# Kernel tuning notes

Hardware: AMD Instinct MI355X
Metric: run time of the kernel (lower is better)

Reference implementation:

```python
import jax, jax.numpy as jnp
import numpy as np

B, T, DM, H, DH, P = 8, 512, 1024, 16, 64, 3584


def rotate_half(x):
    x1, x2 = x[..., : x.shape[-1] // 2], x[..., x.shape[-1] // 2 :]
    return jnp.concatenate([-x2, x1], axis=-1)


def setup_inputs() -> dict:
    key = jax.random.key(0)
    ks = jax.random.split(key, 16)
    x_new = jax.random.normal(ks[0], (B, T, DM), dtype=jnp.float32)
    # realistic RoPE tables for positions [P, P+T)
    inv_freq = 1.0 / (10000.0 ** (jnp.arange(0, DH, 2, dtype=jnp.float32) / DH))
    pos = jnp.arange(P, P + T, dtype=jnp.float32)
    freqs = pos[:, None] * inv_freq[None, :]  # [T, DH/2]
    emb = jnp.concatenate([freqs, freqs], axis=-1)  # [T, DH]
    rotary_cos = jnp.cos(emb)[None, None]  # [1,1,T,DH]
    rotary_sin = jnp.sin(emb)[None, None]
    past_k = jax.random.normal(ks[1], (B, H, P, DH), dtype=jnp.float32)
    past_v = jax.random.normal(ks[2], (B, H, P, DH), dtype=jnp.float32)
    past_lengths = jax.random.randint(ks[3], (B,), 0, P + 1, dtype=jnp.int32)
    new_token_counts = jax.random.randint(ks[4], (B,), 1, T + 1, dtype=jnp.int32)
    valid_new_mask = jnp.arange(T)[None, :] < new_token_counts[:, None]  # [B,T] bool
    s = 0.02
    Wq = jax.random.normal(ks[5], (DM, DM), dtype=jnp.float32) * s
    Wk = jax.random.normal(ks[6], (DM, DM), dtype=jnp.float32) * s
    Wv = jax.random.normal(ks[7], (DM, DM), dtype=jnp.float32) * s
    Wo = jax.random.normal(ks[8], (DM, DM), dtype=jnp.float32) * s
    bq = jax.random.normal(ks[9], (DM,), dtype=jnp.float32) * s
    bk = jax.random.normal(ks[10], (DM,), dtype=jnp.float32) * s
    bv = jax.random.normal(ks[11], (DM,), dtype=jnp.float32) * s
    bo = jax.random.normal(ks[12], (DM,), dtype=jnp.float32) * s
    return dict(x_new=x_new, rotary_cos=rotary_cos, rotary_sin=rotary_sin,
                past_k=past_k, past_v=past_v, past_lengths=past_lengths,
                valid_new_mask=valid_new_mask, new_token_counts=new_token_counts,
                Wq=Wq, bq=bq, Wk=Wk, bk=bk, Wv=Wv, bv=bv, Wo=Wo, bo=bo)


def reference(x_new, rotary_cos, rotary_sin, past_k, past_v, past_lengths,
              valid_new_mask, new_token_counts, Wq, bq, Wk, bk, Wv, bv, Wo, bo):
    b, t, _ = x_new.shape
    # projections -> [B,H,T,DH]
    def proj(W, bias):
        y = x_new @ W + bias
        return y.reshape(b, t, H, DH).transpose(0, 2, 1, 3)
    q = proj(Wq, bq)
    k_new = proj(Wk, bk)
    v_new = proj(Wv, bv)
    # RoPE on q and new keys
    cos = rotary_cos.astype(q.dtype)
    sin = rotary_sin.astype(q.dtype)
    q = q * cos + rotate_half(q) * sin
    k_new = k_new * cos + rotate_half(k_new) * sin
    # zero out padded new tokens (applied to q, k_new, v_new as in original)
    vmask = valid_new_mask[:, None, :, None].astype(q.dtype)
    q = q * vmask
    k_new = k_new * vmask
    v_new = v_new * vmask
    # trim/mask past cache per sample
    trimmed_past = jnp.clip(past_lengths, 0, P)
    pmask = (jnp.arange(P)[None, :] < trimmed_past[:, None])[:, None, :, None].astype(q.dtype)
    pk = past_k.astype(q.dtype) * pmask
    pv = past_v.astype(q.dtype) * pmask
    k_total = jnp.concatenate([pk, k_new], axis=2)  # [B,H,P+T,DH]
    v_total = jnp.concatenate([pv, v_new], axis=2)
    total_lengths = trimmed_past + new_token_counts  # [B]
    # key validity mask over concatenated axis: positions < total_lengths
    valid_keys = jnp.arange(P + t)[None, :] < total_lengths[:, None]  # [B,S]
    scale = 1.0 / jnp.sqrt(jnp.asarray(DH, dtype=q.dtype))
    scores = jnp.einsum('bhqd,bhkd->bhqk', q, k_total) * scale  # [B,H,T,S]
    neg = jnp.asarray(-1e9, dtype=scores.dtype)
    scores = jnp.where(valid_keys[:, None, None, :], scores, neg)
    attn = jax.nn.softmax(scores, axis=-1)
    out = jnp.einsum('bhqk,bhkd->bhqd', attn, v_total)  # [B,H,T,DH]
    out = out.transpose(0, 2, 1, 3).reshape(b, t, DM)
    out = out @ Wo + bo
    out = out * valid_new_mask[:, :, None].astype(out.dtype)
    return out
```

## Files before the change

### kernel.cpp

```cpp
#include <hip/hip_runtime.h>


typedef unsigned short u16;
typedef unsigned int   u32;
typedef float  f32x4  __attribute__((ext_vector_type(4)));
typedef __bf16 bf16x8 __attribute__((ext_vector_type(8)));

#define DEV static __device__ __forceinline__

constexpr int NP = 3584;

DEV u16 bf16rn(float f){
  u32 u = __float_as_uint(f);
  return (u16)((u + 0x7fffu + ((u >> 16) & 1u)) >> 16);
}
DEV float bf2f(u16 h){ return __uint_as_float((u32)h << 16); }
DEV void split2(float f, u16 &h, u16 &l){ h = bf16rn(f); l = bf16rn(f - bf2f(h)); }

DEV f32x4 mfma16(bf16x8 a, bf16x8 b, f32x4 c){
  return __builtin_amdgcn_mfma_f32_16x16x32_bf16(a, b, c, 0, 0, 0);
}

DEV ushort4 cvt4(float4 v){
  ushort4 h; h.x=bf16rn(v.x); h.y=bf16rn(v.y); h.z=bf16rn(v.z); h.w=bf16rn(v.w); return h;
}

DEV void gload_lds16(const u16* g, u16* l){
  __builtin_amdgcn_global_load_lds((const __attribute__((address_space(1))) void*)g,
                                   (__attribute__((address_space(3))) void*)l, 16, 0, 0);
}

__global__ __launch_bounds__(256) void k_split_x(const float* __restrict__ x,
                                                 u16* __restrict__ xh, u16* __restrict__ xl){
  int i = blockIdx.x * 256 + threadIdx.x;
  float4 v = ((const float4*)x)[i];
  u16 h0,l0,h1,l1,h2,l2,h3,l3;
  split2(v.x,h0,l0); split2(v.y,h1,l1); split2(v.z,h2,l2); split2(v.w,h3,l3);
  ushort4 hv; hv.x=h0; hv.y=h1; hv.z=h2; hv.w=h3;
  ushort4 lv; lv.x=l0; lv.y=l1; lv.z=l2; lv.w=l3;
  ((ushort4*)xh)[i] = hv; ((ushort4*)xl)[i] = lv;
}

__global__ __launch_bounds__(256) void k_wsplit(const float* __restrict__ w0, const float* __restrict__ w1,
                                                const float* __restrict__ w2, const float* __restrict__ w3,
                                                u16* __restrict__ Wth, u16* __restrict__ Wtl){
  __shared__ float tl[64][65];
  int z = blockIdx.z;
  const float* W = (z==0) ? w0 : (z==1) ? w1 : (z==2) ? w2 : w3;
  u16* oh = Wth + (size_t)z * (1024*1024);
  u16* ol = Wtl + (size_t)z * (1024*1024);
  int n0 = blockIdx.x*64, k0 = blockIdx.y*64;
  int tid = threadIdx.x;
  #pragma unroll
  for (int i=0;i<16;++i){
    int idx = i*256 + tid; int rr = idx >> 6, cc = idx & 63;
    tl[rr][cc] = W[(size_t)(k0+rr)*1024 + n0 + cc];
  }
  __syncthreads();
  #pragma unroll
  for (int i=0;i<16;++i){
    int idx = i*256 + tid; int rr = idx >> 6, cc = idx & 63;
    u16 h,l; split2(tl[cc][rr], h, l);
    size_t o = (size_t)(n0+rr)*1024 + k0 + cc;
    oh[o] = h; ol[o] = l;
  }
}

__global__ __launch_bounds__(256) void k_qkv(
    const u16* __restrict__ xh, const u16* __restrict__ xl,
    const u16* __restrict__ Wth, const u16* __restrict__ Wtl,
    const float* __restrict__ bq, const float* __restrict__ bk, const float* __restrict__ bv,
    const float* __restrict__ rcos, const float* __restrict__ rsin,
    const int* __restrict__ cnts,
    u16* __restrict__ qh, u16* __restrict__ ql,
    u16* __restrict__ knt, u16* __restrict__ vnt)
{
  int zi = blockIdx.z;
  int n0 = blockIdx.x * 128, m0 = blockIdx.y * 128;
  int b = m0 >> 9, t0 = m0 & 511;
  int cnt = cnts[b];
  if (t0 >= cnt) return;
  const u16* Bh = Wth + (size_t)zi * (1024*1024);
  const u16* Bl = Wtl + (size_t)zi * (1024*1024);
  const float* bias = (zi==0) ? bq : (zi==1) ? bk : bv;

  __shared__ u16 sA[2][128*40];
  __shared__ u16 sB[2][128*40];

  int tid = threadIdx.x, lane = tid & 63, wid = tid >> 6;
  int r = lane & 15, quad = lane >> 4;
  int wm = (wid >> 1) * 64, wn = (wid & 1) * 64;

  const f32x4 fz = {0.f,0.f,0.f,0.f};
  f32x4 acc[4][4];
  #pragma unroll
  for (int i=0;i<4;++i){
    #pragma unroll
    for (int j=0;j<4;++j) acc[i][j] = fz;
  }

  int srow = tid >> 2, sc8 = (tid & 3) * 8;

  for (int kt = 0; kt < 32; ++kt){
    int kb = kt * 32;
    __syncthreads();
    {
      size_t ga  = (size_t)(m0 + srow) * 1024 + kb + sc8;
      size_t gb  = (size_t)(n0 + srow) * 1024 + kb + sc8;
      int lo = srow*40 + sc8, lo2 = lo + 64*40;
      *(uint4*)&sA[0][lo]  = *(const uint4*)&xh[ga];
      *(uint4*)&sA[1][lo]  = *(const uint4*)&xl[ga];
      *(uint4*)&sB[0][lo]  = *(const uint4*)&Bh[gb];
      *(uint4*)&sB[1][lo]  = *(const uint4*)&Bl[gb];
      *(uint4*)&sA[0][lo2] = *(const uint4*)&xh[ga + 64*1024];
      *(uint4*)&sA[1][lo2] = *(const uint4*)&xl[ga + 64*1024];
      *(uint4*)&sB[0][lo2] = *(const uint4*)&Bh[gb + 64*1024];
      *(uint4*)&sB[1][lo2] = *(const uint4*)&Bl[gb + 64*1024];
    }
    __syncthreads();
    bf16x8 ah[4], al[4], bh8[4], bl8[4];
    #pragma unroll
    for (int mf=0; mf<4; ++mf){
      int off = (wm + mf*16 + r)*40 + quad*8;
      ah[mf] = *(const bf16x8*)&sA[0][off];
      al[mf] = *(const bf16x8*)&sA[1][off];
    }
    #pragma unroll
    for (int nf=0; nf<4; ++nf){
      int off = (wn + nf*16 + r)*40 + quad*8;
      bh8[nf] = *(const bf16x8*)&sB[0][off];
      bl8[nf] = *(const bf16x8*)&sB[1][off];
    }
    #pragma unroll
    for (int mf=0; mf<4; ++mf){
      #pragma unroll
      for (int nf=0; nf<4; ++nf){
        acc[mf][nf] = mfma16(ah[mf], bh8[nf], acc[mf][nf]);
        acc[mf][nf] = mfma16(al[mf], bh8[nf], acc[mf][nf]);
        acc[mf][nf] = mfma16(ah[mf], bl8[nf], acc[mf][nf]);
      }
    }
  }

  float vals[4][4][4];
  #pragma unroll
  for (int mf=0;mf<4;++mf){
    #pragma unroll
    for (int nf=0;nf<4;++nf){
      float bb = bias[n0 + wn + nf*16 + r];
      #pragma unroll
      for (int e=0;e<4;++e) vals[mf][nf][e] = acc[mf][nf][e] + bb;
    }
  }
  if (zi < 2){
    #pragma unroll
    for (int mf=0;mf<4;++mf){
      #pragma unroll
      for (int e=0;e<4;++e){
        int t = t0 + wm + mf*16 + quad*4 + e;
        #pragma unroll
        for (int nf=0;nf<2;++nf){
          int d = nf*16 + r;
          float c1 = rcos[t*64 + d],      s1 = rsin[t*64 + d];
          float c2 = rcos[t*64 + d + 32], s2 = rsin[t*64 + d + 32];
          float x1 = vals[mf][nf][e], x2 = vals[mf][nf+2][e];
          vals[mf][nf][e]   = x1*c1 - x2*s1;
          vals[mf][nf+2][e] = x2*c2 + x1*s2;
        }
      }
    }
  }
  #pragma unroll
  for (int mf=0;mf<4;++mf){
    #pragma unroll
    for (int e=0;e<4;++e){
      int t = t0 + wm + mf*16 + quad*4 + e;
      float msk = (t < cnt) ? 1.f : 0.f;
      #pragma unroll
      for (int nf=0;nf<4;++nf){
        int gc = n0 + wn + nf*16 + r;
        int head = gc >> 6, d = gc & 63;
        float v = vals[mf][nf][e] * msk;
        u16 hh, ll; split2(v, hh, ll);
        size_t bh8t = (size_t)(b*16 + head)*8;
        if (zi == 0){
          size_t o = ((size_t)(b*16 + head)*512 + t)*64 + d;
          qh[o] = hh; ql[o] = ll;
        } else if (zi == 1){
          size_t o = ((bh8t + (t>>6))*64 + (t&63))*64 + (d ^ ((t&7)<<3));
          knt[o] = hh;
        } else {
          size_t o = ((bh8t + (t>>6))*64 + d)*64 + ((t&63) ^ ((d&7)<<3));
          vnt[o] = hh;
        }
      }
    }
  }
}

__global__ __launch_bounds__(256) void k_conv(
    const float* __restrict__ pk, const float* __restrict__ pv,
    const int* __restrict__ plen,
    u16* __restrict__ ckh, u16* __restrict__ cvt)
{
  int t = blockIdx.x, h = blockIdx.y, b = blockIdx.z;
  int Lp = min(max(plen[b], 0), NP);
  int jend = min(((Lp + 63) >> 6) << 6, NP);
  if (t*64 >= jend) return;
  int tid = threadIdx.x;
  int bh = b*16 + h;
  int row = tid >> 2, cg = (tid & 3) * 16;
  int jj = t*64 + row;
  size_t src = ((size_t)bh*NP + jj)*64;

  __shared__ float tl[64][65];

  float4 kv4[4], vv4[4];
  #pragma unroll
  for (int i=0;i<4;++i){
    kv4[i] = *(const float4*)&pk[src + cg + i*4];
    vv4[i] = *(const float4*)&pv[src + cg + i*4];
  }
  if (jj >= Lp){
    float4 z4 = {0.f,0.f,0.f,0.f};
    #pragma unroll
    for (int i=0;i<4;++i){ kv4[i]=z4; vv4[i]=z4; }
  }
  size_t kdst = ((size_t)bh*NP + jj)*64;
  #pragma unroll
  for (int i=0;i<4;++i){
    int c4 = cg + i*4;
    *(ushort4*)&ckh[kdst + (c4 ^ ((jj&7)<<3))] = cvt4(kv4[i]);
  }
  #pragma unroll
  for (int i=0;i<4;++i){
    tl[row][cg+i*4+0] = vv4[i].x;
    tl[row][cg+i*4+1] = vv4[i].y;
    tl[row][cg+i*4+2] = vv4[i].z;
    tl[row][cg+i*4+3] = vv4[i].w;
  }
  __syncthreads();
  int d = tid >> 2, jg = (tid & 3) * 16;
  size_t vdst = (((size_t)bh*56 + t)*64 + d)*64;
  #pragma unroll
  for (int i=0;i<4;++i){
    int j4 = jg + i*4;
    ushort4 hv;
    hv.x = bf16rn(tl[j4+0][d]);
    hv.y = bf16rn(tl[j4+1][d]);
    hv.z = bf16rn(tl[j4+2][d]);
    hv.w = bf16rn(tl[j4+3][d]);
    *(ushort4*)&cvt[vdst + (j4 ^ ((d&7)<<3))] = hv;
  }
}

__global__ __launch_bounds__(256,3) void k_attn(
    const u16* __restrict__ qh_, const u16* __restrict__ ql_,
    const u16* __restrict__ knt, const u16* __restrict__ vnt,
    const u16* __restrict__ ckh, const u16* __restrict__ cvt,
    const int* __restrict__ plen, const int* __restrict__ cnts,
    int S, float* __restrict__ pl, float* __restrict__ pO)
{
  int qt = blockIdx.x, h = blockIdx.y;
  int zb = blockIdx.z;
  int b = zb / S, s = zb - b * S;
  int cnt = cnts[b];
  int q0 = qt * 128;
  if (q0 >= cnt) return;
  int Lp = min(max(plen[b], 0), NP);
  int TL = Lp + cnt;
  int Ln = max(0, TL - NP);
  int jend = min(((Lp + 63) >> 6) << 6, NP);
  int minTLP = min(TL, NP);
  int Zar = max(0, minTLP - jend);
  int npast = jend >> 6, nnew = (Ln + 63) >> 6;
  int Tt = npast + nnew;
  int TLu = min(TL, jend) + Ln;
  int qsp = (Tt + S - 1) / S;
  int it0 = s * qsp, it1 = min(Tt, it0 + qsp);
  bool hasZ = (s == 0 && Zar > 0);
  if (it0 >= it1 && !hasZ) return;

  __shared__ __align__(16) u16 sK [2][4096];
  __shared__ __align__(16) u16 sVT[2][4096];
  __shared__ __align__(16) u16 sP [4][2048];

  int tid = threadIdx.x, lane = tid & 63, wid = tid >> 6;
  int r = lane & 15, quad = lane >> 4;
  int wm0 = wid * 32;
  int bh = b*16 + h;

  bf16x8 Qh[2][2], Ql[2][2];
  size_t qbase = ((size_t)bh*512 + q0 + wm0) * 64;
  #pragma unroll
  for (int mf=0;mf<2;++mf){
    #pragma unroll
    for (int ks=0;ks<2;++ks){
      size_t o = qbase + (size_t)(mf*16 + r)*64 + ks*32 + quad*8;
      Qh[mf][ks] = *(const bf16x8*)&qh_[o];
      Ql[mf][ks] = *(const bf16x8*)&ql_[o];
    }
  }

  const f32x4 fz = {0.f,0.f,0.f,0.f};
  f32x4 O[2][4];
  float lsum[2][4];
  #pragma unroll
  for (int mf=0;mf<2;++mf){
    #pragma unroll
    for (int e=0;e<4;++e) lsum[mf][e] = 0.f;
    #pragma unroll
    for (int nf=0;nf<4;++nf) O[mf][nf] = fz;
  }

  const float kscale = 0.125f * 1.44269504088896340736f;
  int ub = wid * 512;

  auto stage = [&](int pp, int it){
    const u16* ks; const u16* vs;
    if (it < npast){
      ks = ckh + ((size_t)bh*NP + (size_t)it*64)*64;
      vs = cvt + ((size_t)bh*56 + it)*4096;
    } else {
      ks = knt + ((size_t)bh*8 + (it - npast))*4096;
      vs = vnt + ((size_t)bh*8 + (it - npast))*4096;
    }
    gload_lds16(ks + ub + lane*8,        &sK [pp][ub]);
    gload_lds16(ks + ub + 2048 + lane*8, &sK [pp][ub + 2048]);
    gload_lds16(vs + ub + lane*8,        &sVT[pp][ub]);
    gload_lds16(vs + ub + 2048 + lane*8, &sVT[pp][ub + 2048]);
  };

  int p = 0;
  if (it0 < it1) stage(0, it0);
  __syncthreads();

  for (int it = it0; it < it1; ++it){
    if (it + 1 < it1) stage(p^1, it + 1);

    f32x4 Sc[2][4];
    #pragma unroll
    for (int mf=0;mf<2;++mf){
      #pragma unroll
      for (int jf=0;jf<4;++jf) Sc[mf][jf] = fz;
    }
    #pragma unroll
    for (int ks=0;ks<2;++ks){
      #pragma unroll
      for (int jf=0;jf<4;++jf){
        int jr = jf*16 + r;
        int off = jr*64 + ((ks*32 + quad*8) ^ ((jr&7)<<3));
        bf16x8 kbh = *(const bf16x8*)&sK[p][off];
        #pragma unroll
        for (int mf=0;mf<2;++mf){
          Sc[mf][jf] = mfma16(Qh[mf][ks], kbh, Sc[mf][jf]);
          Sc[mf][jf] = mfma16(Ql[mf][ks], kbh, Sc[mf][jf]);
        }
      }
    }

    int jlim = TLu - it*64;
    #pragma unroll
    for (int mf=0;mf<2;++mf){
      #pragma unroll
      for (int e=0;e<4;++e){
        int row = mf*16 + quad*4 + e;
        int sw = ((row>>2)&7) << 3;
        float ls = 0.f;
        #pragma unroll
        for (int jf=0;jf<4;++jf){
          float sv = Sc[mf][jf][e] * kscale - 4.0f;
          sv = (jf*16 + r < jlim) ? sv : -3.0e38f;
          float pj = exp2f(sv);
          ls += pj;
          __bf16 pb = (__bf16)pj;
          sP[wid][row*64 + ((jf*16 + r) ^ sw)] = __builtin_bit_cast(u16, pb);
        }
        lsum[mf][e] += ls;
      }
    }
    __syncthreads();

    #pragma unroll
    for (int ks=0;ks<2;++ks){
      bf16x8 pah[2];
      #pragma unroll
      for (int mf=0;mf<2;++mf){
        int row = mf*16 + r;
        pah[mf] = *(const bf16x8*)&sP[wid][row*64 + ((ks*32 + quad*8) ^ (((row>>2)&7)<<3))];
      }
      #pragma unroll
      for (int nf=0;nf<4;++nf){
        int d = nf*16 + r;
        bf16x8 vbh = *(const bf16x8*)&sVT[p][d*64 + ((ks*32 + quad*8) ^ ((d&7)<<3))];
        #pragma unroll
        for (int mf=0;mf<2;++mf){
          O[mf][nf] = mfma16(pah[mf], vbh, O[mf][nf]);
        }
      }
    }
    __syncthreads();
    p ^= 1;
  }

  int pidx = ((b*16 + h)*4 + qt)*S + s;
  float* plr = pl + (size_t)pidx*128;
  float* po  = pO + (size_t)pidx*8192;
  float zadd = (s == 0) ? (float)Zar * 0.0625f : 0.f;
  #pragma unroll
  for (int mf=0;mf<2;++mf){
    #pragma unroll
    for (int e=0;e<4;++e){
      int row = wm0 + mf*16 + quad*4 + e;
      float l = lsum[mf][e];
      l += __shfl_xor(l, 1);
      l += __shfl_xor(l, 2);
      l += __shfl_xor(l, 4);
      l += __shfl_xor(l, 8);
      if (r == 0) plr[row] = l + zadd;
      #pragma unroll
      for (int nf=0;nf<4;++nf) po[row*64 + nf*16 + r] = O[mf][nf][e];
    }
  }
}

__global__ __launch_bounds__(256) void k_reduce(
    const float* __restrict__ pl, const float* __restrict__ pO,
    const int* __restrict__ plen, const int* __restrict__ cnts,
    int S, u16* __restrict__ aoh, u16* __restrict__ aol)
{
  int qt = blockIdx.x, h = blockIdx.y, b = blockIdx.z;
  int cnt = cnts[b]; int q0 = qt*128;
  if (q0 >= cnt) return;
  int Lp = min(max(plen[b], 0), NP);
  int TL = Lp + cnt;
  int Ln = max(0, TL - NP);
  int jend = min(((Lp + 63) >> 6) << 6, NP);
  int minTLP = min(TL, NP);
  int Zar = max(0, minTLP - jend);
  int npast = jend >> 6, nnew = (Ln + 63) >> 6;
  int Tt = npast + nnew;
  int qsp = (Tt + S - 1) / S;

  int tid = threadIdx.x;
  int row = tid >> 1, c0 = (tid & 1) * 32;
  int base = ((b*16 + h)*4 + qt)*S;

  float L = 0.f;
  float acc[32];
  #pragma unroll
  for (int i=0;i<32;++i) acc[i] = 0.f;
  for (int s2=0;s2<S;++s2){
    bool act = (s2*qsp < Tt) || (s2 == 0 && Zar > 0);
    if (!act) continue;
    L += pl[(size_t)(base+s2)*128 + row];
    const float4* po = (const float4*)(pO + (size_t)(base+s2)*8192 + row*64 + c0);
    #pragma unroll
    for (int i=0;i<8;++i){
      float4 v = po[i];
      acc[4*i+0] += v.x; acc[4*i+1] += v.y; acc[4*i+2] += v.z; acc[4*i+3] += v.w;
    }
  }
  float inv = 1.f / L;
  size_t o = ((size_t)b*512 + q0 + row)*1024 + h*64 + c0;
  #pragma unroll
  for (int i=0;i<8;++i){
    ushort4 hv, lv;
    u16 hh, ll;
    split2(acc[4*i+0]*inv, hh, ll); hv.x=hh; lv.x=ll;
    split2(acc[4*i+1]*inv, hh, ll); hv.y=hh; lv.y=ll;
    split2(acc[4*i+2]*inv, hh, ll); hv.z=hh; lv.z=ll;
    split2(acc[4*i+3]*inv, hh, ll); hv.w=hh; lv.w=ll;
    *(ushort4*)&aoh[o + 4*i] = hv;
    *(ushort4*)&aol[o + 4*i] = lv;
  }
}

__global__ __launch_bounds__(256) void k_oproj(
    const u16* __restrict__ ah_, const u16* __restrict__ al_,
    const u16* __restrict__ Wth, const u16* __restrict__ Wtl,
    const float* __restrict__ bo, const int* __restrict__ cnts,
    float* __restrict__ out)
{
  int n0 = blockIdx.x * 128, m0 = blockIdx.y * 128;
  int b = m0 >> 9, t0 = m0 & 511;
  int cnt = cnts[b];
  int tid = threadIdx.x;
  if (t0 >= cnt){
    float4 z4 = {0.f,0.f,0.f,0.f};
    #pragma unroll
    for (int i=0;i<16;++i){
      int v = tid + i*256;
      int row = v >> 5, c4 = (v & 31) * 4;
      *(float4*)&out[(size_t)(m0+row)*1024 + n0 + c4] = z4;
    }
    return;
  }
  const u16* Bh = Wth + 3ull*1024*1024;
  const u16* Bl = Wtl + 3ull*1024*1024;

  __shared__ u16 sA[2][128*40];
  __shared__ u16 sB[2][128*40];

  int lane = tid & 63, wid = tid >> 6;
  int r = lane & 15, quad = lane >> 4;
  int wm = (wid >> 1) * 64, wn = (wid & 1) * 64;

  const f32x4 fz = {0.f,0.f,0.f,0.f};
  f32x4 acc[4][4];
  #pragma unroll
  for (int i=0;i<4;++i){
    #pragma unroll
    for (int j=0;j<4;++j) acc[i][j] = fz;
  }

  int srow = tid >> 2, sc8 = (tid & 3) * 8;

  for (int kt = 0; kt < 32; ++kt){
    int kb = kt * 32;
    __syncthreads();
    {
      size_t ga  = (size_t)(m0 + srow) * 1024 + kb + sc8;
      size_t gb  = (size_t)(n0 + srow) * 1024 + kb + sc8;
      int lo = srow*40 + sc8, lo2 = lo + 64*40;
      *(uint4*)&sA[0][lo]  = *(const uint4*)&ah_[ga];
      *(uint4*)&sA[1][lo]  = *(const uint4*)&al_[ga];
      *(uint4*)&sB[0][lo]  = *(const uint4*)&Bh[gb];
      *(uint4*)&sB[1][lo]  = *(const uint4*)&Bl[gb];
      *(uint4*)&sA[0][lo2] = *(const uint4*)&ah_[ga + 64*1024];
      *(uint4*)&sA[1][lo2] = *(const uint4*)&al_[ga + 64*1024];
      *(uint4*)&sB[0][lo2] = *(const uint4*)&Bh[gb + 64*1024];
      *(uint4*)&sB[1][lo2] = *(const uint4*)&Bl[gb + 64*1024];
    }
    __syncthreads();
    bf16x8 ah8[4], al8[4], bh8[4], bl8[4];
    #pragma unroll
    for (int mf=0; mf<4; ++mf){
      int off = (wm + mf*16 + r)*40 + quad*8;
      ah8[mf] = *(const bf16x8*)&sA[0][off];
      al8[mf] = *(const bf16x8*)&sA[1][off];
    }
    #pragma unroll
    for (int nf=0; nf<4; ++nf){
      int off = (wn + nf*16 + r)*40 + quad*8;
      bh8[nf] = *(const bf16x8*)&sB[0][off];
      bl8[nf] = *(const bf16x8*)&sB[1][off];
    }
    #pragma unroll
    for (int mf=0; mf<4; ++mf){
      #pragma unroll
      for (int nf=0; nf<4; ++nf){
        acc[mf][nf] = mfma16(ah8[mf], bh8[nf], acc[mf][nf]);
        acc[mf][nf] = mfma16(al8[mf], bh8[nf], acc[mf][nf]);
        acc[mf][nf] = mfma16(ah8[mf], bl8[nf], acc[mf][nf]);
      }
    }
  }

  #pragma unroll
  for (int mf=0;mf<4;++mf){
    #pragma unroll
    for (int e=0;e<4;++e){
      int t = t0 + wm + mf*16 + quad*4 + e;
      float msk = (t < cnt) ? 1.f : 0.f;
      int row = m0 + wm + mf*16 + quad*4 + e;
      #pragma unroll
      for (int nf=0;nf<4;++nf){
        int gc = n0 + wn + nf*16 + r;
        out[(size_t)row*1024 + gc] = (acc[mf][nf][e] + bo[gc]) * msk;
      }
    }
  }
}

extern "C" void kernel_launch(void* const* d_in, const int* in_sizes, int n_in,
                              void* d_out, int out_size, void* d_ws, size_t ws_size,
                              hipStream_t stream) {
  (void)in_sizes; (void)n_in; (void)out_size;
  const float* x    = (const float*)d_in[0];
  const float* rcos = (const float*)d_in[1];
  const float* rsin = (const float*)d_in[2];
  const float* pk   = (const float*)d_in[3];
  const float* pv   = (const float*)d_in[4];
  const int*   plen = (const int*)d_in[5];
  const int*   cnts = (const int*)d_in[7];
  const float* Wq = (const float*)d_in[8];
  const float* bq = (const float*)d_in[9];
  const float* Wk = (const float*)d_in[10];
  const float* bk = (const float*)d_in[11];
  const float* Wv = (const float*)d_in[12];
  const float* bv = (const float*)d_in[13];
  const float* Wo = (const float*)d_in[14];
  const float* bo = (const float*)d_in[15];
  float* out = (float*)d_out;

  char* w = (char*)d_ws;
  const size_t MB = 1ull << 20;
  u16* Wth = (u16*)(w + 0*MB);
  u16* Wtl = (u16*)(w + 8*MB);
  u16* qh  = (u16*)(w + 16*MB);
  u16* ql  = (u16*)(w + 24*MB);
  u16* knt = (u16*)(w + 32*MB);
  u16* vnt = (u16*)(w + 40*MB);
  u16* ckh = (u16*)(w + 48*MB);
  u16* xh  = (u16*)(w + 48*MB);
  u16* xl  = (u16*)(w + 56*MB);
  u16* cvt = (u16*)(w + 104*MB);
  float* pl = (float*)(w + 160*MB);
  float* pO = (float*)(w + 162*MB);
  u16* aoh = xh;
  u16* aol = xl;

  int S = (int)((ws_size - 162*MB) / (16*MB));
  if (S > 8) S = 8;
  if (S < 1) S = 1;

  k_split_x<<<dim3(4096), dim3(256), 0, stream>>>(x, xh, xl);
  k_wsplit<<<dim3(16,16,4), dim3(256), 0, stream>>>(Wq, Wk, Wv, Wo, Wth, Wtl);
  k_qkv<<<dim3(8,32,3), dim3(256), 0, stream>>>(xh, xl, Wth, Wtl, bq, bk, bv,
                                                rcos, rsin, cnts,
                                                qh, ql, knt, vnt);
  k_conv<<<dim3(56,16,8), dim3(256), 0, stream>>>(pk, pv, plen, ckh, cvt);
  k_attn<<<dim3(4,16,8*S), dim3(256), 0, stream>>>(qh, ql, knt, vnt, ckh, cvt,
                                                   plen, cnts, S, pl, pO);
  k_reduce<<<dim3(4,16,8), dim3(256), 0, stream>>>(pl, pO, plen, cnts, S, aoh, aol);
  k_oproj<<<dim3(8,32), dim3(256), 0, stream>>>(aoh, aol, Wth, Wtl, bo, cnts, out);
}
```

Baseline: 583.5 us.

## Double-buffer QKV and output-projection GEMMs with direct global-to-LDS loads and block swizzle

The QKV and output-projection GEMM kernels now stage tiles with direct global-to-LDS loads (gload_lds16) into double-buffered shared memory. The next K tile is prefetched while MFMAs run on the current one, cutting the loop to one barrier per iteration. Block indices are remapped so neighbouring blocks share A/B tiles for better L2 reuse, and launch bounds request 2 blocks per CU. The unpadded 32-element LDS rows may cause bank conflicts on fragment reads, and gload_lds16 is assumed to be defined in the hidden part of the file.

Measured after the change: 554.2 us. -5.0%, faster.

```diff
diff --git a/kernel.cpp b/kernel.cpp
--- a/kernel.cpp
+++ b/kernel.cpp
@@ -66,7 +66,7 @@
   }
 }
 
-__global__ __launch_bounds__(256) void k_qkv(
+__global__ __launch_bounds__(256,2) void k_qkv(
     const u16* __restrict__ xh, const u16* __restrict__ xl,
     const u16* __restrict__ Wth, const u16* __restrict__ Wtl,
     const float* __restrict__ bq, const float* __restrict__ bk, const float* __restrict__ bv,
@@ -76,7 +76,9 @@
     u16* __restrict__ knt, u16* __restrict__ vnt)
 {
   int zi = blockIdx.z;
-  int n0 = blockIdx.x * 128, m0 = blockIdx.y * 128;
+  int bx = blockIdx.x, by = blockIdx.y;
+  int n0 = ((bx & 3)*2 + (by & 1)) * 128;
+  int m0 = ((bx >> 2)*16 + (by >> 1)) * 128;
   int b = m0 >> 9, t0 = m0 & 511;
   int cnt = cnts[b];
   if (t0 >= cnt) return;
@@ -84,8 +86,8 @@
   const u16* Bl = Wtl + (size_t)zi * (1024*1024);
   const float* bias = (zi==0) ? bq : (zi==1) ? bk : bv;
 
-  __shared__ u16 sA[2][128*40];
-  __shared__ u16 sB[2][128*40];
+  __shared__ __align__(16) u16 sA[2][2][4096];
+  __shared__ __align__(16) u16 sB[2][2][4096];
 
   int tid = threadIdx.x, lane = tid & 63, wid = tid >> 6;
   int r = lane & 15, quad = lane >> 4;
@@ -99,47 +101,52 @@
     for (int j=0;j<4;++j) acc[i][j] = fz;
   }
 
-  int srow = tid >> 2, sc8 = (tid & 3) * 8;
+  int sc = wid * 2;
+
+  auto stage = [&](int p, int kt){
+    int kb = kt * 32;
+    #pragma unroll
+    for (int c=0;c<2;++c){
+      int s   = (sc + c)*64 + lane;
+      int row = s >> 2;
+      int cg8 = (s & 3) * 8;
+      size_t ga = (size_t)(m0 + row)*1024 + kb + cg8;
+      size_t gb = (size_t)(n0 + row)*1024 + kb + cg8;
+      int lo = (sc + c)*512;
+      gload_lds16(&xh[ga], &sA[p][0][lo]);
+      gload_lds16(&xl[ga], &sA[p][1][lo]);
+      gload_lds16(&Bh[gb], &sB[p][0][lo]);
+      gload_lds16(&Bl[gb], &sB[p][1][lo]);
+    }
+  };
+
+  stage(0, 0);
+  __syncthreads();
 
   for (int kt = 0; kt < 32; ++kt){
-    int kb = kt * 32;
+    int cur = kt & 1;
+    if (kt + 1 < 32) stage(cur ^ 1, kt + 1);
+
+    bf16x8 ah[4], al[4];
+    #pragma unroll
+    for (int mf=0; mf<4; ++mf){
+      int off = (wm + mf*16 + r)*32 + quad*8;
+      ah[mf] = *(const bf16x8*)&sA[cur][0][off];
+      al[mf] = *(const bf16x8*)&sA[cur][1][off];
+    }
+    #pragma unroll
+    for (int nf=0; nf<4; ++nf){
+      int off = (wn + nf*16 + r)*32 + quad*8;
+      bf16x8 bh8 = *(const bf16x8*)&sB[cur][0][off];
+      bf16x8 bl8 = *(const bf16x8*)&sB[cur][1][off];
+      #pragma unroll
+      for (int mf=0; mf<4; ++mf){
+        acc[mf][nf] = mfma16(ah[mf], bh8, acc[mf][nf]);
+        acc[mf][nf] = mfma16(al[mf], bh8, acc[mf][nf]);
+        acc[mf][nf] = mfma16(ah[mf], bl8, acc[mf][nf]);
+      }
+    }
     __syncthreads();
-    {
-      size_t ga  = (size_t)(m0 + srow) * 1024 + kb + sc8;
-      size_t gb  = (size_t)(n0 + srow) * 1024 + kb + sc8;
-      int lo = srow*40 + sc8, lo2 = lo + 64*40;
-      *(uint4*)&sA[0][lo]  = *(const uint4*)&xh[ga];
-      *(uint4*)&sA[1][lo]  = *(const uint4*)&xl[ga];
-      *(uint4*)&sB[0][lo]  = *(const uint4*)&Bh[gb];
-      *(uint4*)&sB[1][lo]  = *(const uint4*)&Bl[gb];
-      *(uint4*)&sA[0][lo2] = *(const uint4*)&xh[ga + 64*1024];
-      *(uint4*)&sA[1][lo2] = *(const uint4*)&xl[ga + 64*1024];
-      *(uint4*)&sB[0][lo2] = *(const uint4*)&Bh[gb + 64*1024];
-      *(uint4*)&sB[1][lo2] = *(const uint4*)&Bl[gb + 64*1024];
-    }
-    __syncthreads();
-    bf16x8 ah[4], al[4], bh8[4], bl8[4];
-    #pragma unroll
-    for (int mf=0; mf<4; ++mf){
-      int off = (wm + mf*16 + r)*40 + quad*8;
-      ah[mf] = *(const bf16x8*)&sA[0][off];
-      al[mf] = *(const bf16x8*)&sA[1][off];
-    }
-    #pragma unroll
-    for (int nf=0; nf<4; ++nf){
-      int off = (wn + nf*16 + r)*40 + quad*8;
-      bh8[nf] = *(const bf16x8*)&sB[0][off];
-      bl8[nf] = *(const bf16x8*)&sB[1][off];
-    }
-    #pragma unroll
-    for (int mf=0; mf<4; ++mf){
-      #pragma unroll
-      for (int nf=0; nf<4; ++nf){
-        acc[mf][nf] = mfma16(ah[mf], bh8[nf], acc[mf][nf]);
-        acc[mf][nf] = mfma16(al[mf], bh8[nf], acc[mf][nf]);
-        acc[mf][nf] = mfma16(ah[mf], bl8[nf], acc[mf][nf]);
-      }
-    }
   }
 
   float vals[4][4][4];
@@ -476,13 +483,15 @@
   }
 }
 
-__global__ __launch_bounds__(256) void k_oproj(
+__global__ __launch_bounds__(256,2) void k_oproj(
     const u16* __restrict__ ah_, const u16* __restrict__ al_,
     const u16* __restrict__ Wth, const u16* __restrict__ Wtl,
     const float* __restrict__ bo, const int* __restrict__ cnts,
     float* __restrict__ out)
 {
-  int n0 = blockIdx.x * 128, m0 = blockIdx.y * 128;
+  int bx = blockIdx.x, by = blockIdx.y;
+  int n0 = ((bx & 3)*2 + (by & 1)) * 128;
+  int m0 = ((bx >> 2)*16 + (by >> 1)) * 128;
   int b = m0 >> 9, t0 = m0 & 511;
   int cnt = cnts[b];
   int tid = threadIdx.x;
@@ -499,8 +508,8 @@
   const u16* Bh = Wth + 3ull*1024*1024;
   const u16* Bl = Wtl + 3ull*1024*1024;
 
-  __shared__ u16 sA[2][128*40];
-  __shared__ u16 sB[2][128*40];
+  __shared__ __align__(16) u16 sA[2][2][4096];
+  __shared__ __align__(16) u16 sB[2][2][4096];
 
   int lane = tid & 63, wid = tid >> 6;
   int r = lane & 15, quad = lane >> 4;
@@ -514,47 +523,52 @@
     for (int j=0;j<4;++j) acc[i][j] = fz;
   }
 
-  int srow = tid >> 2, sc8 = (tid & 3) * 8;
+  int sc = wid * 2;
+
+  auto stage = [&](int p, int kt){
+    int kb = kt * 32;
+    #pragma unroll
+    for (int c=0;c<2;++c){
+      int s   = (sc + c)*64 + lane;
+      int row = s >> 2;
+      int cg8 = (s & 3) * 8;
+      size_t ga = (size_t)(m0 + row)*1024 + kb + cg8;
+      size_t gb = (size_t)(n0 + row)*1024 + kb + cg8;
+      int lo = (sc + c)*512;
+      gload_lds16(&ah_[ga], &sA[p][0][lo]);
+      gload_lds16(&al_[ga], &sA[p][1][lo]);
+      gload_lds16(&Bh[gb],  &sB[p][0][lo]);
+      gload_lds16(&Bl[gb],  &sB[p][1][lo]);
+    }
+  };
+
+  stage(0, 0);
+  __syncthreads();
 
   for (int kt = 0; kt < 32; ++kt){
-    int kb = kt * 32;
+    int cur = kt & 1;
+    if (kt + 1 < 32) stage(cur ^ 1, kt + 1);
+
+    bf16x8 ah8[4], al8[4];
+    #pragma unroll
+    for (int mf=0; mf<4; ++mf){
+      int off = (wm + mf*16 + r)*32 + quad*8;
+      ah8[mf] = *(const bf16x8*)&sA[cur][0][off];
+      al8[mf] = *(const bf16x8*)&sA[cur][1][off];
+    }
+    #pragma unroll
+    for (int nf=0; nf<4; ++nf){
+      int off = (wn + nf*16 + r)*32 + quad*8;
+      bf16x8 bh8 = *(const bf16x8*)&sB[cur][0][off];
+      bf16x8 bl8 = *(const bf16x8*)&sB[cur][1][off];
+      #pragma unroll
+      for (int mf=0; mf<4; ++mf){
+        acc[mf][nf] = mfma16(ah8[mf], bh8, acc[mf][nf]);
+        acc[mf][nf] = mfma16(al8[mf], bh8, acc[mf][nf]);
+        acc[mf][nf] = mfma16(ah8[mf], bl8, acc[mf][nf]);
+      }
+    }
     __syncthreads();
-    {
-      size_t ga  = (size_t)(m0 + srow) * 1024 + kb + sc8;
-      size_t gb  = (size_t)(n0 + srow) * 1024 + kb + sc8;
-      int lo = srow*40 + sc8, lo2 = lo + 64*40;
-      *(uint4*)&sA[0][lo]  = *(const uint4*)&ah_[ga];
-      *(uint4*)&sA[1][lo]  = *(const uint4*)&al_[ga];
-      *(uint4*)&sB[0][lo]  = *(const uint4*)&Bh[gb];
-      *(uint4*)&sB[1][lo]  = *(const uint4*)&Bl[gb];
-      *(uint4*)&sA[0][lo2] = *(const uint4*)&ah_[ga + 64*1024];
-      *(uint4*)&sA[1][lo2] = *(const uint4*)&al_[ga + 64*1024];
-      *(uint4*)&sB[0][lo2] = *(const uint4*)&Bh[gb + 64*1024];
-      *(uint4*)&sB[1][lo2] = *(const uint4*)&Bl[gb + 64*1024];
-    }
-    __syncthreads();
-    bf16x8 ah8[4], al8[4], bh8[4], bl8[4];
-    #pragma unroll
-    for (int mf=0; mf<4; ++mf){
-      int off = (wm + mf*16 + r)*40 + quad*8;
-      ah8[mf] = *(const bf16x8*)&sA[0][off];
-      al8[mf] = *(const bf16x8*)&sA[1][off];
-    }
-    #pragma unroll
-    for (int nf=0; nf<4; ++nf){
-      int off = (wn + nf*16 + r)*40 + quad*8;
-      bh8[nf] = *(const bf16x8*)&sB[0][off];
-      bl8[nf] = *(const bf16x8*)&sB[1][off];
-    }
-    #pragma unroll
-    for (int mf=0; mf<4; ++mf){
-      #pragma unroll
-      for (int nf=0; nf<4; ++nf){
-        acc[mf][nf] = mfma16(ah8[mf], bh8[nf], acc[mf][nf]);
-        acc[mf][nf] = mfma16(al8[mf], bh8[nf], acc[mf][nf]);
-        acc[mf][nf] = mfma16(ah8[mf], bl8[nf], acc[mf][nf]);
-      }
-    }
   }
 
   #pragma unroll
```
